# Performance work log

Hardware: AMD Instinct MI355X
Metric: run time of the kernel (lower is better)

## Reference

```python
import jax, jax.numpy as jnp
import numpy as np

B, N, F, H, HEADS = 2, 256, 64, 64, 4
C = HEADS * H  # n_coefficients (coefficients_mlp is Identity => must equal n_heads*hidden)
EPS = 1e-5
INF = 1e5


def _lin(key, fan_in, fan_out, bias=True):
    k1, k2 = jax.random.split(key)
    w = jax.random.normal(k1, (fan_in, fan_out), jnp.float32) * (1.0 / np.sqrt(fan_in))
    if bias:
        b = jax.random.normal(k2, (fan_out,), jnp.float32) * 0.01
        return w, b
    return w


def setup_inputs() -> dict:
    key = jax.random.key(0)
    ks = jax.random.split(key, 16)
    inp = dict(
        h=jax.random.normal(ks[0], (B, N, F), jnp.float32),
        x=jax.random.normal(ks[1], (B, N, 3), jnp.float32),
        v=jax.random.normal(ks[2], (B, N, 3), jnp.float32),
    )
    inp['edge_w1'], inp['edge_b1'] = _lin(ks[3], 2 * F + 1, H)
    inp['edge_w2'], inp['edge_b2'] = _lin(ks[4], H, H)
    inp['sem_w'], inp['sem_b'] = _lin(ks[5], H, HEADS)
    inp['post_w1'], inp['post_b1'] = _lin(ks[6], C, H)
    inp['post_w2'], inp['post_b2'] = _lin(ks[7], H, H)
    inp['node_w1'], inp['node_b1'] = _lin(ks[8], C + H + F, H)
    inp['node_w2'], inp['node_b2'] = _lin(ks[9], H, F)
    inp['vel_w1'], inp['vel_b1'] = _lin(ks[10], F, H)
    inp['vel_w2'] = _lin(ks[11], H, 1, bias=False) * 0.001  # xavier gain=0.001 analogue
    inp['vmix_w'] = _lin(ks[12], C, 1, bias=False)[:, 0]
    inp['log_gamma'] = -jnp.log(jnp.linspace(1.0, 5.0, HEADS)).astype(jnp.float32)
    return inp


def reference(h, x, v, edge_w1, edge_b1, edge_w2, edge_b2, sem_w, sem_b,
              post_w1, post_b1, post_w2, post_b2, node_w1, node_b1,
              node_w2, node_b2, vel_w1, vel_b1, vel_w2, vmix_w, log_gamma):
    silu = jax.nn.silu
    n = h.shape[-2]
    eye = jnp.eye(n, dtype=h.dtype)[:, :, None]  # [N,N,1] diagonal mask

    # pairwise geometry: entry [i,j] = x_j - x_i
    x_minus_xt = x[..., None, :, :] - x[..., :, None, :]                # [B,N,N,3]
    x_norm = jnp.sqrt((x_minus_xt ** 2).sum(-1, keepdims=True) + EPS)   # [B,N,N,1]

    # pairwise node-feature concat (h_j, h_i) + distance -> edge MLP
    h_j = jnp.broadcast_to(h[..., None, :, :], (B, n, n, F))
    h_i = jnp.broadcast_to(h[..., :, None, :], (B, n, n, F))
    h_cat = jnp.concatenate([h_j, h_i, x_norm], axis=-1)                # [B,N,N,2F+1]
    h_e_mtx = silu(silu(h_cat @ edge_w1 + edge_b1) @ edge_w2 + edge_b2)  # [B,N,N,H]

    # euclidean attention: softmin over j of gamma*dist, diagonal masked out
    dist = (x_norm + INF * eye) * jnp.exp(log_gamma)                    # [B,N,N,heads]
    euclid_att = jax.nn.softmax(-dist, axis=-2)
    # semantic attention: LeakyReLU(0.2) logits, diagonal masked, softmax over j
    sem = jax.nn.leaky_relu(h_e_mtx @ sem_w + sem_b, 0.2) - INF * eye
    sem_att = jax.nn.softmax(sem, axis=-2)
    comb_att = jax.nn.softmax(euclid_att * sem_att, axis=-2)            # [B,N,N,heads]

    # attention-weighted edge features, flattened over (H, heads)
    h_e_att = (h_e_mtx[..., :, None] * comb_att[..., None, :]).reshape(B, n, n, C)

    # spatial attention (coefficients_mlp is Identity)
    unit = x_minus_xt / (x_norm + EPS)                                  # [B,N,N,3]
    # combinations.mean(dim=-3) without materializing [B,N,N,C,3]
    comb_sum = jnp.einsum('bijc,bijd->bicd', h_e_att, unit) / n         # [B,N,C,3]
    comb_norm = (comb_sum ** 2).sum(-1)                                 # [B,N,C]
    h_comb = silu(silu(comb_norm @ post_w1 + post_b1) @ post_w2 + post_b2)

    # delta_v = mean_j (v_mixing over C of combinations)
    delta_v = jnp.einsum('bijc,c,bijd->bid', h_e_att, vmix_w, unit) / n  # [B,N,3]

    h_agg = h_e_att.sum(axis=-2)                                        # sum over j -> [B,N,C]
    out = jnp.concatenate([h, h_agg, h_comb], axis=-1)
    out = silu(silu(out @ node_w1 + node_b1) @ node_w2 + node_b2)
    h_new = h + out                                                     # residual

    # coordinate / velocity update
    v_scale = silu(h_new @ vel_w1 + vel_b1) @ vel_w2                    # [B,N,1]
    v_new = delta_v + v_scale * v
    x_new = x + v_new
    return h_new, x_new, v_new
```

## Files before the change

kernel.cpp:

```cpp
#include <hip/hip_runtime.h>
#include <hip/hip_bf16.h>
#include <math.h>

#define EPSV 1e-5f
#define INFV 1e5f

typedef short bf16x8 __attribute__((ext_vector_type(8)));
typedef float f32x4 __attribute__((ext_vector_type(4)));

__device__ __forceinline__ float rcp_f(float x) { return __builtin_amdgcn_rcpf(x); }
__device__ __forceinline__ float silu_f(float v) { return v * rcp_f(1.0f + __expf(-v)); }

__device__ __forceinline__ unsigned short f2bf(float f) {
  unsigned int u = __float_as_uint(f);
  u = (u + 0x7fffu + ((u >> 16) & 1u)) >> 16;
  return (unsigned short)u;
}
__device__ __forceinline__ float bf2f(unsigned short h) {
  return __uint_as_float(((unsigned int)h) << 16);
}
__device__ __forceinline__ unsigned int pkbf(float a, float b) {
  float2 f2; f2.x = a; f2.y = b;
  __hip_bfloat162 t = __float22bfloat162_rn(f2);
  unsigned int u;
  __builtin_memcpy(&u, &t, 4);
  return u;
}

__device__ __forceinline__ void gemm64(const unsigned short* TH, const unsigned short* E2T,
                                       int w, int l15, int quad, f32x4 acc[4][4]) {
#pragma unroll
  for (int tr = 0; tr < 4; ++tr)
#pragma unroll
    for (int tc = 0; tc < 4; ++tc)
      acc[tr][tc] = (f32x4){0.f, 0.f, 0.f, 0.f};
#pragma unroll
  for (int ms = 0; ms < 64; ms += 32) {
    bf16x8 af[4], bfr[4];
#pragma unroll
    for (int tr = 0; tr < 4; ++tr)
      af[tr] = *reinterpret_cast<const bf16x8*>(&TH[(64 * w + 16 * tr + l15) * 72 + ms + quad * 8]);
#pragma unroll
    for (int tc = 0; tc < 4; ++tc)
      bfr[tc] = *reinterpret_cast<const bf16x8*>(&E2T[(16 * tc + l15) * 72 + ms + quad * 8]);
#pragma unroll
    for (int tr = 0; tr < 4; ++tr)
#pragma unroll
      for (int tc = 0; tc < 4; ++tc)
        acc[tr][tc] = __builtin_amdgcn_mfma_f32_16x16x32_bf16(af[tr], bfr[tc], acc[tr][tc], 0, 0, 0);
  }
}

__global__ __launch_bounds__(256, 3) void k_all(
    const float* __restrict__ h, const float* __restrict__ x, const float* __restrict__ v,
    const float* __restrict__ ew1, const float* __restrict__ eb1,
    const float* __restrict__ ew2, const float* __restrict__ eb2,
    const float* __restrict__ semw, const float* __restrict__ semb,
    const float* __restrict__ pw1, const float* __restrict__ pb1,
    const float* __restrict__ pw2, const float* __restrict__ pb2,
    const float* __restrict__ nw1, const float* __restrict__ nb1,
    const float* __restrict__ nw2, const float* __restrict__ nb2,
    const float* __restrict__ vw1, const float* __restrict__ vb1,
    const float* __restrict__ vw2, const float* __restrict__ vmix,
    const float* __restrict__ lgam, float* __restrict__ out) {

  __shared__ __align__(16) unsigned short TH[256 * 72];
  __shared__ __align__(16) char E2u[9472];
  __shared__ __align__(16) float4 unit_l[256];
  __shared__ float addk[64];
  __shared__ float w1dk[64];
  __shared__ __align__(16) float bms[256];

  unsigned short* E2T = (unsigned short*)E2u;
  float*  sd    = (float*)(E2u + 1280);
  float4* cat_l = (float4*)E2u;
  float*  cn_l  = (float*)(E2u + 4096);
  float*  hag_l = (float*)(E2u + 5120);
  float4* scS = (float4*)bms;
  float4* scP = (float4*)bms + 8;
  float4* scD = (float4*)bms + 12;
  float*  dvs = bms + 64;

  const int bi  = blockIdx.x;
  const int i   = bi & 255;
  const int b0  = bi & ~255;
  const int tid = threadIdx.x;
  const int j   = tid;
  const int bj  = b0 | j;

  const float xi0 = x[bi * 3 + 0], xi1 = x[bi * 3 + 1], xi2 = x[bi * 3 + 2];
  const float dx = x[bj * 3 + 0] - xi0;
  const float dy = x[bj * 3 + 1] - xi1;
  const float dz = x[bj * 3 + 2] - xi2;
  const float dn = sqrtf(dx * dx + dy * dy + dz * dz + EPSV);
  const float invn = rcp_f(dn + EPSV);
  const float ux = dx * invn, uy = dy * invn, uz = dz * invn;
  unit_l[j] = make_float4(ux, uy, uz, dn);

  {
    const float4* hb4 = reinterpret_cast<const float4*>(h + (size_t)b0 * 64);
#pragma unroll
    for (int q = 0; q < 16; ++q) {
      int idx = q * 256 + tid;
      float4 f4 = hb4[idx];
      int row = idx >> 4, c4 = idx & 15;
      uint2 pk;
      pk.x = pkbf(f4.x, f4.y);
      pk.y = pkbf(f4.z, f4.w);
      *reinterpret_cast<uint2*>(&TH[row * 72 + c4 * 4]) = pk;
    }
  }
#pragma unroll
  for (int q = 0; q < 16; ++q) {
    int idx = q * 256 + tid;
    E2T[(idx & 63) * 72 + (idx >> 6)] = f2bf(ew1[idx]);
  }
  {
    int s = tid >> 6, k = tid & 63;
    const float* hrow = h + (size_t)bi * 64;
    float bp = 0.f;
#pragma unroll
    for (int f2 = 0; f2 < 16; ++f2) {
      int f = s * 16 + f2;
      bp += hrow[f] * ew1[(64 + f) * 64 + k];
    }
    bms[s * 64 + k] = bp;
  }
  __syncthreads();
  if (tid < 64) {
    addk[tid] = eb1[tid] + bms[tid] + bms[64 + tid] + bms[128 + tid] + bms[192 + tid];
    w1dk[tid] = ew1[128 * 64 + tid];
  }

  const int lid  = tid & 63;
  const int w    = tid >> 6;
  const int l15  = lid & 15;
  const int quad = lid >> 4;

  f32x4 acc[4][4];
  gemm64(TH, E2T, w, l15, quad, acc);
  __syncthreads();

#pragma unroll
  for (int tc = 0; tc < 4; ++tc) {
    float ak = addk[16 * tc + l15];
    float wd = w1dk[16 * tc + l15];
#pragma unroll
    for (int tr = 0; tr < 4; ++tr)
#pragma unroll
      for (int r = 0; r < 4; ++r) {
        int row = 64 * w + 16 * tr + quad * 4 + r;
        float val = silu_f(acc[tr][tc][r] + ak + unit_l[row].w * wd);
        TH[row * 72 + 16 * tc + l15] = f2bf(val);
      }
  }
#pragma unroll
  for (int q = 0; q < 16; ++q) {
    int idx = q * 256 + tid;
    E2T[(idx & 63) * 72 + (idx >> 6)] = f2bf(ew2[idx]);
  }
  __syncthreads();

  gemm64(TH, E2T, w, l15, quad, acc);
  __syncthreads();

#pragma unroll
  for (int tc = 0; tc < 4; ++tc) {
    float b2 = eb2[16 * tc + l15];
#pragma unroll
    for (int tr = 0; tr < 4; ++tr)
#pragma unroll
      for (int r = 0; r < 4; ++r) {
        int row = 64 * w + 16 * tr + quad * 4 + r;
        TH[row * 72 + 16 * tc + l15] = f2bf(silu_f(acc[tr][tc][r] + b2));
      }
  }
#pragma unroll
  for (int q = 0; q < 2; ++q) {
    int idx = q * 256 + tid;
    int n = idx >> 6, kk = idx & 63;
    float wv = (n < 4) ? semw[kk * 4 + n] : vmix[kk * 4 + (n - 4)];
    E2T[n * 72 + kk] = f2bf(wv);
  }
  __syncthreads();

  f32x4 acc3[4];
  {
#pragma unroll
    for (int tr = 0; tr < 4; ++tr) acc3[tr] = (f32x4){0.f, 0.f, 0.f, 0.f};
#pragma unroll
    for (int ms = 0; ms < 64; ms += 32) {
      bf16x8 b3 = *reinterpret_cast<const bf16x8*>(&E2T[l15 * 72 + ms + quad * 8]);
#pragma unroll
      for (int tr = 0; tr < 4; ++tr) {
        bf16x8 a3 = *reinterpret_cast<const bf16x8*>(&TH[(64 * w + 16 * tr + l15) * 72 + ms + quad * 8]);
        acc3[tr] = __builtin_amdgcn_mfma_f32_16x16x32_bf16(a3, b3, acc3[tr], 0, 0, 0);
      }
    }
  }
  if (l15 < 8) {
#pragma unroll
    for (int tr = 0; tr < 4; ++tr)
#pragma unroll
      for (int r = 0; r < 4; ++r)
        sd[(64 * w + 16 * tr + quad * 4 + r) * 8 + l15] = acc3[tr][r];
  }
  __syncthreads();

  float4 s01 = *reinterpret_cast<const float4*>(sd + j * 8);
  float4 s23 = *reinterpret_cast<const float4*>(sd + j * 8 + 4);
  float4 sbv = *reinterpret_cast<const float4*>(semb);
  const float diag = (j == i) ? INFV : 0.0f;
  float4 sl;
  sl.x = s01.x + sbv.x; sl.y = s01.y + sbv.y; sl.z = s01.z + sbv.z; sl.w = s01.w + sbv.w;
  sl.x = ((sl.x > 0.f) ? sl.x : 0.2f * sl.x) - diag;
  sl.y = ((sl.y > 0.f) ? sl.y : 0.2f * sl.y) - diag;
  sl.z = ((sl.z > 0.f) ? sl.z : 0.2f * sl.z) - diag;
  sl.w = ((sl.w > 0.f) ? sl.w : 0.2f * sl.w) - diag;

  float4 lg = *reinterpret_cast<const float4*>(lgam);
  const float dni = dn + diag;
  float4 e_eu = make_float4(__expf(-dni * __expf(lg.x)), __expf(-dni * __expf(lg.y)),
                            __expf(-dni * __expf(lg.z)), __expf(-dni * __expf(lg.w)));
  float4 e_sem = make_float4(__expf(sl.x), __expf(sl.y), __expf(sl.z), __expf(sl.w));

  float4 a8 = e_eu, b8 = e_sem;
#pragma unroll
  for (int off = 32; off >= 1; off >>= 1) {
    a8.x += __shfl_xor(a8.x, off); a8.y += __shfl_xor(a8.y, off);
    a8.z += __shfl_xor(a8.z, off); a8.w += __shfl_xor(a8.w, off);
    b8.x += __shfl_xor(b8.x, off); b8.y += __shfl_xor(b8.y, off);
    b8.z += __shfl_xor(b8.z, off); b8.w += __shfl_xor(b8.w, off);
  }
  if (lid == 0) { scS[w] = a8; scS[4 + w] = b8; }
  __syncthreads();
  float4 Se, Ss;
  {
    float4 r0 = scS[0], r1 = scS[1], r2 = scS[2], r3 = scS[3];
    Se = make_float4(r0.x + r1.x + r2.x + r3.x, r0.y + r1.y + r2.y + r3.y,
                     r0.z + r1.z + r2.z + r3.z, r0.w + r1.w + r2.w + r3.w);
    float4 s0 = scS[4], s1 = scS[5], s2 = scS[6], s3 = scS[7];
    Ss = make_float4(s0.x + s1.x + s2.x + s3.x, s0.y + s1.y + s2.y + s3.y,
                     s0.z + s1.z + s2.z + s3.z, s0.w + s1.w + s2.w + s3.w);
  }

  float4 p = make_float4((e_eu.x * rcp_f(Se.x)) * (e_sem.x * rcp_f(Ss.x)),
                         (e_eu.y * rcp_f(Se.y)) * (e_sem.y * rcp_f(Ss.y)),
                         (e_eu.z * rcp_f(Se.z)) * (e_sem.z * rcp_f(Ss.z)),
                         (e_eu.w * rcp_f(Se.w)) * (e_sem.w * rcp_f(Ss.w)));
  float4 ep = make_float4(__expf(p.x), __expf(p.y), __expf(p.z), __expf(p.w));
  float4 sp8 = ep;
#pragma unroll
  for (int off = 32; off >= 1; off >>= 1) {
    sp8.x += __shfl_xor(sp8.x, off); sp8.y += __shfl_xor(sp8.y, off);
    sp8.z += __shfl_xor(sp8.z, off); sp8.w += __shfl_xor(sp8.w, off);
  }
  if (lid == 0) scP[w] = sp8;
  __syncthreads();
  float4 Sp;
  {
    float4 r0 = scP[0], r1 = scP[1], r2 = scP[2], r3 = scP[3];
    Sp = make_float4(r0.x + r1.x + r2.x + r3.x, r0.y + r1.y + r2.y + r3.y,
                     r0.z + r1.z + r2.z + r3.z, r0.w + r1.w + r2.w + r3.w);
  }
  float4 catt = make_float4(ep.x * rcp_f(Sp.x), ep.y * rcp_f(Sp.y),
                            ep.z * rcp_f(Sp.z), ep.w * rcp_f(Sp.w));
  cat_l[j] = catt;

  float s = catt.x * s23.x + catt.y * s23.y + catt.z * s23.z + catt.w * s23.w;
  float dvx = s * ux, dvy = s * uy, dvz = s * uz;
#pragma unroll
  for (int off = 32; off >= 1; off >>= 1) {
    dvx += __shfl_xor(dvx, off); dvy += __shfl_xor(dvy, off); dvz += __shfl_xor(dvz, off);
  }
  if (lid == 0) scD[w] = make_float4(dvx, dvy, dvz, 0.f);
  __syncthreads();
  if (j == 0) {
    float4 r0 = scD[0], r1 = scD[1], r2 = scD[2], r3 = scD[3];
    const float inv = 1.0f / 256.0f;
    dvs[0] = (r0.x + r1.x + r2.x + r3.x) * inv;
    dvs[1] = (r0.y + r1.y + r2.y + r3.y) * inv;
    dvs[2] = (r0.z + r1.z + r2.z + r3.z) * inv;
  }

  {
    const int kk = lid & 15;
    const int jq = lid >> 4;
    const int k  = 16 * w + kk;
    float agg[4] = {0.f, 0.f, 0.f, 0.f};
    float ax[4]  = {0.f, 0.f, 0.f, 0.f};
    float ay[4]  = {0.f, 0.f, 0.f, 0.f};
    float az[4]  = {0.f, 0.f, 0.f, 0.f};
#pragma unroll 4
    for (int jr2 = 0; jr2 < 64; ++jr2) {
      int jj = jq * 64 + ((jr2 + 4 * jq) & 63);
      float hev = bf2f(TH[jj * 72 + k]);
      float4 ca = cat_l[jj];
      float4 u  = unit_l[jj];
      float w0 = hev * ca.x, w1 = hev * ca.y, w2 = hev * ca.z, w3 = hev * ca.w;
      agg[0] += w0; agg[1] += w1; agg[2] += w2; agg[3] += w3;
      ax[0] += w0 * u.x; ay[0] += w0 * u.y; az[0] += w0 * u.z;
      ax[1] += w1 * u.x; ay[1] += w1 * u.y; az[1] += w1 * u.z;
      ax[2] += w2 * u.x; ay[2] += w2 * u.y; az[2] += w2 * u.z;
      ax[3] += w3 * u.x; ay[3] += w3 * u.y; az[3] += w3 * u.z;
    }
#pragma unroll
    for (int off = 16; off <= 32; off <<= 1) {
#pragma unroll
      for (int hd = 0; hd < 4; ++hd) {
        agg[hd] += __shfl_xor(agg[hd], off);
        ax[hd]  += __shfl_xor(ax[hd], off);
        ay[hd]  += __shfl_xor(ay[hd], off);
        az[hd]  += __shfl_xor(az[hd], off);
      }
    }
    if (jq == 0) {
      const float inv = 1.0f / 256.0f;
#pragma unroll
      for (int hd = 0; hd < 4; ++hd) {
        float cx = ax[hd] * inv, cy = ay[hd] * inv, cz = az[hd] * inv;
        cn_l[k * 4 + hd]  = cx * cx + cy * cy + cz * cz;
        hag_l[k * 4 + hd] = agg[hd];
      }
    }
  }
  __syncthreads();

  if (w == 0) {
    const int k = tid;
    float* shr = (float*)TH;

    float a = 0.f;
#pragma unroll 16
    for (int m = 0; m < 256; ++m) a += cn_l[m] * pw1[m * 64 + k];
    float m1 = silu_f(pb1[k] + a);
    shr[k] = m1;

    a = 0.f;
#pragma unroll 16
    for (int m = 0; m < 64; ++m) a += shr[m] * pw2[m * 64 + k];
    float hcomb = silu_f(pb2[k] + a);
    float hrow = h[(size_t)bi * 64 + k];
    shr[64 + k]  = hrow;
    shr[128 + k] = hcomb;

    a = 0.f;
#pragma unroll 16
    for (int m = 0; m < 64; ++m) a += shr[64 + m] * nw1[m * 64 + k];
#pragma unroll 16
    for (int m = 0; m < 256; ++m) a += hag_l[m] * nw1[(64 + m) * 64 + k];
#pragma unroll 16
    for (int m = 0; m < 64; ++m) a += shr[128 + m] * nw1[(320 + m) * 64 + k];
    float n1 = silu_f(nb1[k] + a);
    shr[192 + k] = n1;

    a = 0.f;
#pragma unroll 16
    for (int m = 0; m < 64; ++m) a += shr[192 + m] * nw2[m * 64 + k];
    float hn = hrow + silu_f(nb2[k] + a);
    out[(size_t)bi * 64 + k] = hn;
    shr[256 + k] = hn;

    a = 0.f;
#pragma unroll 16
    for (int m = 0; m < 64; ++m) a += shr[256 + m] * vw1[m * 64 + k];
    float vh = silu_f(vb1[k] + a) * vw2[k];
#pragma unroll
    for (int off = 32; off >= 1; off >>= 1) vh += __shfl_xor(vh, off);

    if (k == 0) {
      const float xi[3] = {xi0, xi1, xi2};
#pragma unroll
      for (int d = 0; d < 3; ++d) {
        float vn = dvs[d] + vh * v[bi * 3 + d];
        out[32768 + bi * 3 + d] = xi[d] + vn;
        out[34304 + bi * 3 + d] = vn;
      }
    }
  }
}

extern "C" void kernel_launch(void* const* d_in, const int* in_sizes, int n_in,
                              void* d_out, int out_size, void* d_ws, size_t ws_size,
                              hipStream_t stream) {
  const float* h    = (const float*)d_in[0];
  const float* x    = (const float*)d_in[1];
  const float* v    = (const float*)d_in[2];
  const float* ew1  = (const float*)d_in[3];
  const float* eb1  = (const float*)d_in[4];
  const float* ew2  = (const float*)d_in[5];
  const float* eb2  = (const float*)d_in[6];
  const float* semw = (const float*)d_in[7];
  const float* semb = (const float*)d_in[8];
  const float* pw1  = (const float*)d_in[9];
  const float* pb1  = (const float*)d_in[10];
  const float* pw2  = (const float*)d_in[11];
  const float* pb2  = (const float*)d_in[12];
  const float* nw1  = (const float*)d_in[13];
  const float* nb1  = (const float*)d_in[14];
  const float* nw2  = (const float*)d_in[15];
  const float* nb2  = (const float*)d_in[16];
  const float* vw1  = (const float*)d_in[17];
  const float* vb1  = (const float*)d_in[18];
  const float* vw2  = (const float*)d_in[19];
  const float* vmix = (const float*)d_in[20];
  const float* lgam = (const float*)d_in[21];
  float* out = (float*)d_out;

  k_all<<<512, 256, 0, stream>>>(h, x, v, ew1, eb1, ew2, eb2, semw, semb,
                                 pw1, pb1, pw2, pb2, nw1, nb1, nw2, nb2,
                                 vw1, vb1, vw2, vmix, lgam, out);
}
```

Before: 128.4 us.

## Process two target nodes per block, sharing the first edge GEMM

Each 512-thread block now handles two query nodes i. The first edge-MLP layer's h_j·W1 product is computed once and reused for both nodes, with only the per-i bias and distance terms added separately. Weight staging for ew1, ew2 and sem/vmix is done up front into separate LDS regions, which removes the mid-kernel restaging syncs. The final per-node MLP's long reductions are split across four waves instead of running serially in one wave. LDS use roughly doubles, which lowers occupancy, and only 256 blocks are launched.

```diff
diff --git a/kernel.cpp b/kernel.cpp
--- a/kernel.cpp
+++ b/kernel.cpp
@@ -27,7 +27,7 @@
   return u;
 }
 
-__device__ __forceinline__ void gemm64(const unsigned short* TH, const unsigned short* E2T,
+__device__ __forceinline__ void gemm64(const unsigned short* A_lds, const unsigned short* B_lds,
                                        int w, int l15, int quad, f32x4 acc[4][4]) {
 #pragma unroll
   for (int tr = 0; tr < 4; ++tr)
@@ -39,10 +39,10 @@
     bf16x8 af[4], bfr[4];
 #pragma unroll
     for (int tr = 0; tr < 4; ++tr)
-      af[tr] = *reinterpret_cast<const bf16x8*>(&TH[(64 * w + 16 * tr + l15) * 72 + ms + quad * 8]);
+      af[tr] = *reinterpret_cast<const bf16x8*>(&A_lds[(64 * w + 16 * tr + l15) * 72 + ms + quad * 8]);
 #pragma unroll
     for (int tc = 0; tc < 4; ++tc)
-      bfr[tc] = *reinterpret_cast<const bf16x8*>(&E2T[(16 * tc + l15) * 72 + ms + quad * 8]);
+      bfr[tc] = *reinterpret_cast<const bf16x8*>(&B_lds[(16 * tc + l15) * 72 + ms + quad * 8]);
 #pragma unroll
     for (int tr = 0; tr < 4; ++tr)
 #pragma unroll
@@ -51,7 +51,7 @@
   }
 }
 
-__global__ __launch_bounds__(256, 3) void k_all(
+__global__ __launch_bounds__(512, 2) void k_all(
     const float* __restrict__ h, const float* __restrict__ x, const float* __restrict__ v,
     const float* __restrict__ ew1, const float* __restrict__ eb1,
     const float* __restrict__ ew2, const float* __restrict__ eb2,
@@ -64,29 +64,44 @@
     const float* __restrict__ vw2, const float* __restrict__ vmix,
     const float* __restrict__ lgam, float* __restrict__ out) {
 
-  __shared__ __align__(16) unsigned short TH[256 * 72];
-  __shared__ __align__(16) char E2u[9472];
-  __shared__ __align__(16) float4 unit_l[256];
-  __shared__ float addk[64];
+  __shared__ __align__(16) unsigned short TH0[256 * 72];
+  __shared__ __align__(16) unsigned short TH1[256 * 72];
+  __shared__ __align__(16) char R0[9216];
+  __shared__ __align__(16) char R1[9216];
+  __shared__ __align__(16) unsigned short E3T[16 * 72];
+  __shared__ __align__(16) float4 unit_l[2][256];
+  __shared__ float addk[2][64];
   __shared__ float w1dk[64];
-  __shared__ __align__(16) float bms[256];
-
-  unsigned short* E2T = (unsigned short*)E2u;
-  float*  sd    = (float*)(E2u + 1280);
-  float4* cat_l = (float4*)E2u;
-  float*  cn_l  = (float*)(E2u + 4096);
-  float*  hag_l = (float*)(E2u + 5120);
-  float4* scS = (float4*)bms;
-  float4* scP = (float4*)bms + 8;
-  float4* scD = (float4*)bms + 12;
-  float*  dvs = bms + 64;
-
-  const int bi  = blockIdx.x;
-  const int i   = bi & 255;
-  const int b0  = bi & ~255;
+  __shared__ __align__(16) float bms[512];
+
+  const int bid = blockIdx.x;
+  const int b   = bid >> 7;
+  const int ip  = bid & 127;
   const int tid = threadIdx.x;
-  const int j   = tid;
-  const int bj  = b0 | j;
+  const int g   = tid >> 8;
+  const int jt  = tid & 255;
+  const int i_g = 2 * ip + g;
+  const int bi  = (b << 8) | i_g;
+  const int bj  = (b << 8) | jt;
+
+  const int w8   = tid >> 6;
+  const int lid  = tid & 63;
+  const int wg   = w8 & 3;
+  const int l15  = lid & 15;
+  const int quad = lid >> 4;
+
+  unsigned short* E2Ta = (unsigned short*)R0;
+  unsigned short* E2Tb = (unsigned short*)R1;
+  unsigned short* THg  = g ? TH1 : TH0;
+  char* Rg = g ? R1 : R0;
+  float*  sd_g  = (float*)Rg;
+  float4* cat_g = (float4*)Rg;
+  float*  cn_g  = (float*)(Rg + 4096);
+  float*  hag_g = (float*)(Rg + 5120);
+  float4* scS   = (float4*)bms + g * 8;
+  float4* scP   = (float4*)bms + 16 + g * 4;
+  float4* scD   = (float4*)bms + 24 + g * 4;
+  float*  dvs_g = bms + 128 + g * 4;
 
   const float xi0 = x[bi * 3 + 0], xi1 = x[bi * 3 + 1], xi2 = x[bi * 3 + 2];
   const float dx = x[bj * 3 + 0] - xi0;
@@ -95,28 +110,38 @@
   const float dn = sqrtf(dx * dx + dy * dy + dz * dz + EPSV);
   const float invn = rcp_f(dn + EPSV);
   const float ux = dx * invn, uy = dy * invn, uz = dz * invn;
-  unit_l[j] = make_float4(ux, uy, uz, dn);
-
-  {
-    const float4* hb4 = reinterpret_cast<const float4*>(h + (size_t)b0 * 64);
-#pragma unroll
-    for (int q = 0; q < 16; ++q) {
-      int idx = q * 256 + tid;
+  unit_l[g][jt] = make_float4(ux, uy, uz, dn);
+
+  {
+    const float4* hb4 = reinterpret_cast<const float4*>(h + (size_t)(b << 8) * 64);
+#pragma unroll
+    for (int q = 0; q < 8; ++q) {
+      int idx = q * 512 + tid;
       float4 f4 = hb4[idx];
       int row = idx >> 4, c4 = idx & 15;
       uint2 pk;
       pk.x = pkbf(f4.x, f4.y);
       pk.y = pkbf(f4.z, f4.w);
-      *reinterpret_cast<uint2*>(&TH[row * 72 + c4 * 4]) = pk;
-    }
-  }
-#pragma unroll
-  for (int q = 0; q < 16; ++q) {
-    int idx = q * 256 + tid;
-    E2T[(idx & 63) * 72 + (idx >> 6)] = f2bf(ew1[idx]);
-  }
-  {
-    int s = tid >> 6, k = tid & 63;
+      *reinterpret_cast<uint2*>(&TH0[row * 72 + c4 * 4]) = pk;
+    }
+  }
+#pragma unroll
+  for (int q = 0; q < 8; ++q) {
+    int idx = q * 512 + tid;
+    E2Ta[(idx & 63) * 72 + (idx >> 6)] = f2bf(ew1[idx]);
+  }
+#pragma unroll
+  for (int q = 0; q < 8; ++q) {
+    int idx = q * 512 + tid;
+    E2Tb[(idx & 63) * 72 + (idx >> 6)] = f2bf(ew2[idx]);
+  }
+  {
+    int n = tid >> 6, kk = tid & 63;
+    E3T[n * 72 + kk] = f2bf((n < 4) ? semw[kk * 4 + n] : vmix[kk * 4 + (n - 4)]);
+    E3T[(8 + n) * 72 + kk] = 0;
+  }
+  {
+    int s = jt >> 6, k = jt & 63;
     const float* hrow = h + (size_t)bi * 64;
     float bp = 0.f;
 #pragma unroll
@@ -124,46 +149,60 @@
       int f = s * 16 + f2;
       bp += hrow[f] * ew1[(64 + f) * 64 + k];
     }
-    bms[s * 64 + k] = bp;
-  }
-  __syncthreads();
-  if (tid < 64) {
-    addk[tid] = eb1[tid] + bms[tid] + bms[64 + tid] + bms[128 + tid] + bms[192 + tid];
-    w1dk[tid] = ew1[128 * 64 + tid];
-  }
-
-  const int lid  = tid & 63;
-  const int w    = tid >> 6;
-  const int l15  = lid & 15;
-  const int quad = lid >> 4;
-
-  f32x4 acc[4][4];
-  gemm64(TH, E2T, w, l15, quad, acc);
+    bms[g * 256 + s * 64 + k] = bp;
+  }
+  __syncthreads();
+  if (tid < 128) {
+    int ii = tid >> 6, k = tid & 63;
+    addk[ii][k] = eb1[k] + bms[ii * 256 + k] + bms[ii * 256 + 64 + k] +
+                  bms[ii * 256 + 128 + k] + bms[ii * 256 + 192 + k];
+  }
+  if (tid < 64) w1dk[tid] = ew1[128 * 64 + tid];
+
+  f32x4 acc1[2][4];
+#pragma unroll
+  for (int tr = 0; tr < 2; ++tr)
+#pragma unroll
+    for (int tc = 0; tc < 4; ++tc)
+      acc1[tr][tc] = (f32x4){0.f, 0.f, 0.f, 0.f};
+#pragma unroll
+  for (int ms = 0; ms < 64; ms += 32) {
+    bf16x8 af[2], bfr[4];
+#pragma unroll
+    for (int tr = 0; tr < 2; ++tr)
+      af[tr] = *reinterpret_cast<const bf16x8*>(&TH0[(32 * w8 + 16 * tr + l15) * 72 + ms + quad * 8]);
+#pragma unroll
+    for (int tc = 0; tc < 4; ++tc)
+      bfr[tc] = *reinterpret_cast<const bf16x8*>(&E2Ta[(16 * tc + l15) * 72 + ms + quad * 8]);
+#pragma unroll
+    for (int tr = 0; tr < 2; ++tr)
+#pragma unroll
+      for (int tc = 0; tc < 4; ++tc)
+        acc1[tr][tc] = __builtin_amdgcn_mfma_f32_16x16x32_bf16(af[tr], bfr[tc], acc1[tr][tc], 0, 0, 0);
+  }
   __syncthreads();
 
 #pragma unroll
   for (int tc = 0; tc < 4; ++tc) {
-    float ak = addk[16 * tc + l15];
-    float wd = w1dk[16 * tc + l15];
-#pragma unroll
-    for (int tr = 0; tr < 4; ++tr)
+    float wd  = w1dk[16 * tc + l15];
+    float ak0 = addk[0][16 * tc + l15];
+    float ak1 = addk[1][16 * tc + l15];
+#pragma unroll
+    for (int tr = 0; tr < 2; ++tr)
 #pragma unroll
       for (int r = 0; r < 4; ++r) {
-        int row = 64 * w + 16 * tr + quad * 4 + r;
-        float val = silu_f(acc[tr][tc][r] + ak + unit_l[row].w * wd);
-        TH[row * 72 + 16 * tc + l15] = f2bf(val);
-      }
-  }
-#pragma unroll
-  for (int q = 0; q < 16; ++q) {
-    int idx = q * 256 + tid;
-    E2T[(idx & 63) * 72 + (idx >> 6)] = f2bf(ew2[idx]);
-  }
-  __syncthreads();
-
-  gemm64(TH, E2T, w, l15, quad, acc);
-  __syncthreads();
-
+        int row = 32 * w8 + 16 * tr + quad * 4 + r;
+        float a = acc1[tr][tc][r];
+        float d0 = unit_l[0][row].w, d1 = unit_l[1][row].w;
+        TH0[row * 72 + 16 * tc + l15] = f2bf(silu_f(a + ak0 + d0 * wd));
+        TH1[row * 72 + 16 * tc + l15] = f2bf(silu_f(a + ak1 + d1 * wd));
+      }
+  }
+  __syncthreads();
+
+  f32x4 acc2[4][4];
+  gemm64(THg, E2Tb, wg, l15, quad, acc2);
+  __syncthreads();
 #pragma unroll
   for (int tc = 0; tc < 4; ++tc) {
     float b2 = eb2[16 * tc + l15];
@@ -171,31 +210,22 @@
     for (int tr = 0; tr < 4; ++tr)
 #pragma unroll
       for (int r = 0; r < 4; ++r) {
-        int row = 64 * w + 16 * tr + quad * 4 + r;
-        TH[row * 72 + 16 * tc + l15] = f2bf(silu_f(acc[tr][tc][r] + b2));
-      }
-  }
-#pragma unroll
-  for (int q = 0; q < 2; ++q) {
-    int idx = q * 256 + tid;
-    int n = idx >> 6, kk = idx & 63;
-    float wv = (n < 4) ? semw[kk * 4 + n] : vmix[kk * 4 + (n - 4)];
-    E2T[n * 72 + kk] = f2bf(wv);
+        int row = 64 * wg + 16 * tr + quad * 4 + r;
+        THg[row * 72 + 16 * tc + l15] = f2bf(silu_f(acc2[tr][tc][r] + b2));
+      }
   }
   __syncthreads();
 
   f32x4 acc3[4];
-  {
-#pragma unroll
-    for (int tr = 0; tr < 4; ++tr) acc3[tr] = (f32x4){0.f, 0.f, 0.f, 0.f};
-#pragma unroll
-    for (int ms = 0; ms < 64; ms += 32) {
-      bf16x8 b3 = *reinterpret_cast<const bf16x8*>(&E2T[l15 * 72 + ms + quad * 8]);
-#pragma unroll
-      for (int tr = 0; tr < 4; ++tr) {
-        bf16x8 a3 = *reinterpret_cast<const bf16x8*>(&TH[(64 * w + 16 * tr + l15) * 72 + ms + quad * 8]);
-        acc3[tr] = __builtin_amdgcn_mfma_f32_16x16x32_bf16(a3, b3, acc3[tr], 0, 0, 0);
-      }
+#pragma unroll
+  for (int tr = 0; tr < 4; ++tr) acc3[tr] = (f32x4){0.f, 0.f, 0.f, 0.f};
+#pragma unroll
+  for (int ms = 0; ms < 64; ms += 32) {
+    bf16x8 b3 = *reinterpret_cast<const bf16x8*>(&E3T[l15 * 72 + ms + quad * 8]);
+#pragma unroll
+    for (int tr = 0; tr < 4; ++tr) {
+      bf16x8 a3 = *reinterpret_cast<const bf16x8*>(&THg[(64 * wg + 16 * tr + l15) * 72 + ms + quad * 8]);
+      acc3[tr] = __builtin_amdgcn_mfma_f32_16x16x32_bf16(a3, b3, acc3[tr], 0, 0, 0);
     }
   }
   if (l15 < 8) {
@@ -203,14 +233,14 @@
     for (int tr = 0; tr < 4; ++tr)
 #pragma unroll
       for (int r = 0; r < 4; ++r)
-        sd[(64 * w + 16 * tr + quad * 4 + r) * 8 + l15] = acc3[tr][r];
-  }
-  __syncthreads();
-
-  float4 s01 = *reinterpret_cast<const float4*>(sd + j * 8);
-  float4 s23 = *reinterpret_cast<const float4*>(sd + j * 8 + 4);
+        sd_g[(64 * wg + 16 * tr + quad * 4 + r) * 8 + l15] = acc3[tr][r];
+  }
+  __syncthreads();
+
+  float4 s01 = *reinterpret_cast<const float4*>(sd_g + jt * 8);
+  float4 s23 = *reinterpret_cast<const float4*>(sd_g + jt * 8 + 4);
   float4 sbv = *reinterpret_cast<const float4*>(semb);
-  const float diag = (j == i) ? INFV : 0.0f;
+  const float diag = (jt == i_g) ? INFV : 0.0f;
   float4 sl;
   sl.x = s01.x + sbv.x; sl.y = s01.y + sbv.y; sl.z = s01.z + sbv.z; sl.w = s01.w + sbv.w;
   sl.x = ((sl.x > 0.f) ? sl.x : 0.2f * sl.x) - diag;
@@ -218,10 +248,10 @@
   sl.z = ((sl.z > 0.f) ? sl.z : 0.2f * sl.z) - diag;
   sl.w = ((sl.w > 0.f) ? sl.w : 0.2f * sl.w) - diag;
 
-  float4 lg = *reinterpret_cast<const float4*>(lgam);
+  float4 lg4 = *reinterpret_cast<const float4*>(lgam);
   const float dni = dn + diag;
-  float4 e_eu = make_float4(__expf(-dni * __expf(lg.x)), __expf(-dni * __expf(lg.y)),
-                            __expf(-dni * __expf(lg.z)), __expf(-dni * __expf(lg.w)));
+  float4 e_eu = make_float4(__expf(-dni * __expf(lg4.x)), __expf(-dni * __expf(lg4.y)),
+                            __expf(-dni * __expf(lg4.z)), __expf(-dni * __expf(lg4.w)));
   float4 e_sem = make_float4(__expf(sl.x), __expf(sl.y), __expf(sl.z), __expf(sl.w));
 
   float4 a8 = e_eu, b8 = e_sem;
@@ -232,7 +262,7 @@
     b8.x += __shfl_xor(b8.x, off); b8.y += __shfl_xor(b8.y, off);
     b8.z += __shfl_xor(b8.z, off); b8.w += __shfl_xor(b8.w, off);
   }
-  if (lid == 0) { scS[w] = a8; scS[4 + w] = b8; }
+  if (lid == 0) { scS[wg] = a8; scS[4 + wg] = b8; }
   __syncthreads();
   float4 Se, Ss;
   {
@@ -255,7 +285,7 @@
     sp8.x += __shfl_xor(sp8.x, off); sp8.y += __shfl_xor(sp8.y, off);
     sp8.z += __shfl_xor(sp8.z, off); sp8.w += __shfl_xor(sp8.w, off);
   }
-  if (lid == 0) scP[w] = sp8;
+  if (lid == 0) scP[wg] = sp8;
   __syncthreads();
   float4 Sp;
   {
@@ -265,7 +295,7 @@
   }
   float4 catt = make_float4(ep.x * rcp_f(Sp.x), ep.y * rcp_f(Sp.y),
                             ep.z * rcp_f(Sp.z), ep.w * rcp_f(Sp.w));
-  cat_l[j] = catt;
+  cat_g[jt] = catt;
 
   float s = catt.x * s23.x + catt.y * s23.y + catt.z * s23.z + catt.w * s23.w;
   float dvx = s * ux, dvy = s * uy, dvz = s * uz;
@@ -273,20 +303,20 @@
   for (int off = 32; off >= 1; off >>= 1) {
     dvx += __shfl_xor(dvx, off); dvy += __shfl_xor(dvy, off); dvz += __shfl_xor(dvz, off);
   }
-  if (lid == 0) scD[w] = make_float4(dvx, dvy, dvz, 0.f);
-  __syncthreads();
-  if (j == 0) {
+  if (lid == 0) scD[wg] = make_float4(dvx, dvy, dvz, 0.f);
+  __syncthreads();
+  if (jt == 0) {
     float4 r0 = scD[0], r1 = scD[1], r2 = scD[2], r3 = scD[3];
     const float inv = 1.0f / 256.0f;
-    dvs[0] = (r0.x + r1.x + r2.x + r3.x) * inv;
-    dvs[1] = (r0.y + r1.y + r2.y + r3.y) * inv;
-    dvs[2] = (r0.z + r1.z + r2.z + r3.z) * inv;
+    dvs_g[0] = (r0.x + r1.x + r2.x + r3.x) * inv;
+    dvs_g[1] = (r0.y + r1.y + r2.y + r3.y) * inv;
+    dvs_g[2] = (r0.z + r1.z + r2.z + r3.z) * inv;
   }
 
   {
     const int kk = lid & 15;
     const int jq = lid >> 4;
-    const int k  = 16 * w + kk;
+    const int k  = 16 * wg + kk;
     float agg[4] = {0.f, 0.f, 0.f, 0.f};
     float ax[4]  = {0.f, 0.f, 0.f, 0.f};
     float ay[4]  = {0.f, 0.f, 0.f, 0.f};
@@ -294,9 +324,9 @@
 #pragma unroll 4
     for (int jr2 = 0; jr2 < 64; ++jr2) {
       int jj = jq * 64 + ((jr2 + 4 * jq) & 63);
-      float hev = bf2f(TH[jj * 72 + k]);
-      float4 ca = cat_l[jj];
-      float4 u  = unit_l[jj];
+      float hev = bf2f(THg[jj * 72 + k]);
+      float4 ca = cat_g[jj];
+      float4 u  = unit_l[g][jj];
       float w0 = hev * ca.x, w1 = hev * ca.y, w2 = hev * ca.z, w3 = hev * ca.w;
       agg[0] += w0; agg[1] += w1; agg[2] += w2; agg[3] += w3;
       ax[0] += w0 * u.x; ay[0] += w0 * u.y; az[0] += w0 * u.z;
@@ -319,51 +349,71 @@
 #pragma unroll
       for (int hd = 0; hd < 4; ++hd) {
         float cx = ax[hd] * inv, cy = ay[hd] * inv, cz = az[hd] * inv;
-        cn_l[k * 4 + hd]  = cx * cx + cy * cy + cz * cz;
-        hag_l[k * 4 + hd] = agg[hd];
-      }
-    }
-  }
-  __syncthreads();
-
-  if (w == 0) {
-    const int k = tid;
-    float* shr = (float*)TH;
+        cn_g[k * 4 + hd]  = cx * cx + cy * cy + cz * cz;
+        hag_g[k * 4 + hd] = agg[hd];
+      }
+    }
+  }
+  __syncthreads();
+
+  {
+    const int k = lid;
+    float* tmpg = (float*)THg;
+    float a1 = 0.f;
+#pragma unroll 16
+    for (int m2 = 0; m2 < 64; ++m2) {
+      int m = 64 * wg + m2;
+      a1 += cn_g[m] * pw1[m * 64 + k];
+    }
+    tmpg[wg * 64 + k] = a1;
+    if (wg == 1 || wg == 2) {
+      float a2 = 0.f;
+      int base = (wg - 1) * 128;
+#pragma unroll 16
+      for (int m2 = 0; m2 < 128; ++m2) {
+        int m = base + m2;
+        a2 += hag_g[m] * nw1[(64 + m) * 64 + k];
+      }
+      tmpg[256 + (wg - 1) * 64 + k] = a2;
+    } else if (wg == 3) {
+      float a2 = 0.f;
+      const float* hrow = h + (size_t)bi * 64;
+#pragma unroll 16
+      for (int m = 0; m < 64; ++m) a2 += hrow[m] * nw1[m * 64 + k];
+      tmpg[384 + k] = a2;
+    }
+  }
+  __syncthreads();
+
+  if (wg == 0) {
+    const int k = lid;
+    float* tmpg = (float*)THg;
+    float* sh2  = tmpg + 512;
+
+    float m1 = silu_f(pb1[k] + tmpg[k] + tmpg[64 + k] + tmpg[128 + k] + tmpg[192 + k]);
+    sh2[k] = m1;
 
     float a = 0.f;
 #pragma unroll 16
-    for (int m = 0; m < 256; ++m) a += cn_l[m] * pw1[m * 64 + k];
-    float m1 = silu_f(pb1[k] + a);
-    shr[k] = m1;
+    for (int m = 0; m < 64; ++m) a += sh2[m] * pw2[m * 64 + k];
+    float hcomb = silu_f(pb2[k] + a);
+    sh2[64 + k] = hcomb;
+
+    a = nb1[k] + tmpg[256 + k] + tmpg[320 + k] + tmpg[384 + k];
+#pragma unroll 16
+    for (int m = 0; m < 64; ++m) a += sh2[64 + m] * nw1[(320 + m) * 64 + k];
+    sh2[128 + k] = silu_f(a);
 
     a = 0.f;
 #pragma unroll 16
-    for (int m = 0; m < 64; ++m) a += shr[m] * pw2[m * 64 + k];
-    float hcomb = silu_f(pb2[k] + a);
-    float hrow = h[(size_t)bi * 64 + k];
-    shr[64 + k]  = hrow;
-    shr[128 + k] = hcomb;
+    for (int m = 0; m < 64; ++m) a += sh2[128 + m] * nw2[m * 64 + k];
+    float hn = h[(size_t)bi * 64 + k] + silu_f(nb2[k] + a);
+    out[(size_t)bi * 64 + k] = hn;
+    sh2[192 + k] = hn;
 
     a = 0.f;
 #pragma unroll 16
-    for (int m = 0; m < 64; ++m) a += shr[64 + m] * nw1[m * 64 + k];
-#pragma unroll 16
-    for (int m = 0; m < 256; ++m) a += hag_l[m] * nw1[(64 + m) * 64 + k];
-#pragma unroll 16
-    for (int m = 0; m < 64; ++m) a += shr[128 + m] * nw1[(320 + m) * 64 + k];
-    float n1 = silu_f(nb1[k] + a);
-    shr[192 + k] = n1;
-
-    a = 0.f;
-#pragma unroll 16
-    for (int m = 0; m < 64; ++m) a += shr[192 + m] * nw2[m * 64 + k];
-    float hn = hrow + silu_f(nb2[k] + a);
-    out[(size_t)bi * 64 + k] = hn;
-    shr[256 + k] = hn;
-
-    a = 0.f;
-#pragma unroll 16
-    for (int m = 0; m < 64; ++m) a += shr[256 + m] * vw1[m * 64 + k];
+    for (int m = 0; m < 64; ++m) a += sh2[192 + m] * vw1[m * 64 + k];
     float vh = silu_f(vb1[k] + a) * vw2[k];
 #pragma unroll
     for (int off = 32; off >= 1; off >>= 1) vh += __shfl_xor(vh, off);
@@ -372,7 +422,7 @@
       const float xi[3] = {xi0, xi1, xi2};
 #pragma unroll
       for (int d = 0; d < 3; ++d) {
-        float vn = dvs[d] + vh * v[bi * 3 + d];
+        float vn = dvs_g[d] + vh * v[bi * 3 + d];
         out[32768 + bi * 3 + d] = xi[d] + vn;
         out[34304 + bi * 3 + d] = vn;
       }
@@ -407,7 +457,7 @@
   const float* lgam = (const float*)d_in[21];
   float* out = (float*)d_out;
 
-  k_all<<<512, 256, 0, stream>>>(h, x, v, ew1, eb1, ew2, eb2, semw, semb,
+  k_all<<<256, 512, 0, stream>>>(h, x, v, ew1, eb1, ew2, eb2, semw, semb,
                                  pw1, pb1, pw2, pb2, nw1, nb1, nw2, nb2,
                                  vw1, vb1, vw2, vmix, lgam, out);
 }
```

Measured after the change: 126.7 us. Within noise of the previous version (-1.3%).
